# Optimization experiments

Measured on AMD Instinct MI355X. Metric: run time of the kernel, lower is better.

Reference implementation:

```python
import jax, jax.numpy as jnp
import numpy as np
from jax import lax

N_C = 1024  # number of FPS centroids (hard-coded in forward)
K = 32      # knn neighbors (hard-coded in forward)


def _fps(x, far0):
    # Faithful to the source: dist is recomputed against ONLY the latest
    # centroid each iteration (the mask/min-update in the source is dead code),
    # then far = argmax(dist).
    B = x.shape[0]
    bidx = jnp.arange(B)

    def step(far, _):
        c = x[bidx, far]                              # [B, C]
        d = jnp.sum((x - c[:, None, :]) ** 2, -1)     # [B, N]
        return jnp.argmax(d, -1), c

    _, cents = lax.scan(step, far0, None, length=N_C)  # cents: [n_c, B, C]
    return jnp.transpose(cents, (1, 0, 2))             # [B, n_c, C]


def _knn_group(x, cent):
    # squared euclidean distances (same argsort order as torch.cdist)
    d2 = (jnp.sum(cent ** 2, -1)[..., None]
          + jnp.sum(x ** 2, -1)[:, None, :]
          - 2.0 * jnp.einsum('bmc,bnc->bmn', cent, x))   # [B, n_c, N]
    _, idx = lax.top_k(-d2, K)                            # [B, n_c, K] smallest dists
    neighbors = jax.vmap(lambda xb, ib: xb[ib])(x, idx)   # [B, n_c, K, C]
    return neighbors


def _conv1x1(h, w, b):
    # 1x1 Conv1d == channel matmul; h: [B, Cin, L], w: [Cout, Cin]
    return jax.nn.relu(jnp.einsum('oi,bil->bol', w, h) + b[None, :, None])


def setup_inputs() -> dict:
    key = jax.random.key(0)
    ks = jax.random.split(key, 20)
    B, N, C = 4, 16384, 3
    num_classes = 3
    p = lambda k, shp: (jax.random.normal(k, shp, jnp.float32) * 0.02)
    return {
        'x': jax.random.normal(ks[0], (B, N, C), jnp.float32),
        'far_init': jax.random.randint(ks[1], (B,), 0, N, jnp.int32),
        'w1': p(ks[2], (64, 3)),    'b1': p(ks[3], (64,)),
        'w2': p(ks[4], (64, 64)),   'b2': p(ks[5], (64,)),
        'w3': p(ks[6], (64, 64)),   'b3': p(ks[7], (64,)),
        'w4': p(ks[8], (128, 64)),  'b4': p(ks[9], (128,)),
        'w5': p(ks[10], (1024, 128)), 'b5': p(ks[11], (1024,)),
        'fw1': p(ks[12], (512, 1024)), 'fb1': p(ks[13], (512,)),
        'fw2': p(ks[14], (256, 512)),  'fb2': p(ks[15], (256,)),
        'fw3': p(ks[16], (num_classes, 256)), 'fb3': p(ks[17], (num_classes,)),
    }


def reference(x, far_init, w1, b1, w2, b2, w3, b3, w4, b4, w5, b5,
              fw1, fb1, fw2, fb2, fw3, fb3):
    B, N, C = x.shape
    cent = _fps(x, far_init)                 # [B, n_c, C]
    neighbors = _knn_group(x, cent)          # [B, n_c, K, C]
    h = jnp.transpose(neighbors, (0, 3, 1, 2)).reshape(B, C, N_C * K)
    h = _conv1x1(h, w1, b1)
    h = _conv1x1(h, w2, b2)
    h = _conv1x1(h, w3, b3)
    h = _conv1x1(h, w4, b4)
    h = _conv1x1(h, w5, b5)                  # [B, 1024, n_c*K]
    g = jnp.max(h, axis=2)                   # global max pool -> [B, 1024]
    g = jax.nn.relu(g @ fw1.T + fb1)
    g = jax.nn.relu(g @ fw2.T + fb2)
    return g @ fw3.T + fb3                   # [B, num_classes]
```

## Files before the change

kernel.cpp:

```cpp
#include <hip/hip_runtime.h>

#define BN  4
#define NPT 16384
#define NCC 1024
#define KNN 32

#define HBINS    2048
#define CCH      2
#define CAND_CAP 768

#define OFF_CCOUNT 0
#define OFF_SCOUNT 64
#define OFF_SBITS  128
#define OFF_POOL   (128 + BN*(NPT/32)*4)
#define OFF_CLIST  (OFF_POOL + BN*NCC*4)
#define OFF_H1     (OFF_CLIST + BN*NCC*4)
#define OFF_H2     (OFF_H1 + BN*512*4)
#define OFF_SLIST  (OFF_H2 + BN*256*4)

typedef short bf16x8 __attribute__((ext_vector_type(8)));
typedef float f32x4  __attribute__((ext_vector_type(4)));
typedef float f32x2  __attribute__((ext_vector_type(2)));

__device__ __forceinline__ short f2bf(float f) {
    unsigned u = __float_as_uint(f);
    return (short)((u + 0x7fffu + ((u >> 16) & 1u)) >> 16);
}
__device__ __forceinline__ bf16x8 cvt8(const float* __restrict__ p) {
    bf16x8 v;
#pragma unroll
    for (int j = 0; j < 8; ++j) v[j] = f2bf(p[j]);
    return v;
}

__global__ __launch_bounds__(1024) void fps_kernel(const float* __restrict__ x,
    const int* __restrict__ far_init, int* __restrict__ clist, int* __restrict__ ccount,
    int* __restrict__ scount, unsigned* __restrict__ sbits, float* __restrict__ pool)
{
#pragma clang fp contract(off)
    const int b = blockIdx.x, t = threadIdx.x;
    __shared__ __align__(16) unsigned char seen[NPT];
    __shared__ unsigned long long slot[3];

    if (t < 512) sbits[b*(NPT/32) + t] = 0u;
    pool[b*NCC + t] = 0.0f;
    if (t == 0) { ccount[b] = 0; scount[b] = 0; }

    const float* xb = x + (size_t)b * NPT * 3;
    f32x2 px[8], py[8], pz[8];
#pragma unroll
    for (int r = 0; r < 8; ++r) {
        int ia = t + ((2*r) << 10), ib = ia + 1024;
        px[r] = f32x2{xb[ia*3+0], xb[ib*3+0]};
        py[r] = f32x2{xb[ia*3+1], xb[ib*3+1]};
        pz[r] = f32x2{xb[ia*3+2], xb[ib*3+2]};
    }
    ((uint4*)seen)[t] = make_uint4(0,0,0,0);
    if (t == 0) { slot[0] = 0ull; slot[1] = 0ull; slot[2] = 0ull; }
    int prev_bx = far_init[b];
    __syncthreads();
    int pbs = __builtin_amdgcn_readfirstlane(prev_bx);
    float cx = xb[pbs*3], cy = xb[pbs*3+1], cz = xb[pbs*3+2];

    int done = 0;
    for (int it = 0; it < NCC-1; ++it) {
        const int p = it % 3;
        const f32x2 cX = {cx, cx}, cY = {cy, cy}, cZ = {cz, cz};
        float best = -1.0f; int bi = 0;
#pragma unroll
        for (int r = 0; r < 8; ++r) {
            f32x2 dx = px[r] - cX;
            f32x2 dy = py[r] - cY;
            f32x2 dz = pz[r] - cZ;
            f32x2 m1 = dx * dx;
            f32x2 m2 = dy * dy;
            f32x2 m3 = dz * dz;
            f32x2 s  = (m1 + m2) + m3;
            int ia = t + ((2*r) << 10);
            if (s.x > best) { best = s.x; bi = ia; }
            if (s.y > best) { best = s.y; bi = ia + 1024; }
        }
#pragma unroll
        for (int m = 1; m < 64; m <<= 1) {
            float od = __shfl_xor(best, m, 64);
            int   oi = __shfl_xor(bi,   m, 64);
            if (od > best || (od == best && oi < bi)) { best = od; bi = oi; }
        }
        if ((t & 63) == 0) {
            unsigned long long pk =
                (((unsigned long long)__float_as_uint(best)) << 32)
                | (unsigned)(NPT - 1 - bi);
            atomicMax(&slot[p], pk);
        }
        if (t == 0) seen[prev_bx] = 1;
        __syncthreads();
        int bx = NPT - 1 - (int)(unsigned)(slot[p] & 0xFFFFFFFFull);
        if (t == 0) slot[(it + 2) % 3] = 0ull;
        if (seen[bx]) { done = 1; break; }
        prev_bx = bx;
        int bxs = __builtin_amdgcn_readfirstlane(bx);
        cx = xb[bxs*3]; cy = xb[bxs*3+1]; cz = xb[bxs*3+2];
    }
    if (!done && t == 0) seen[prev_bx] = 1;
    __syncthreads();
#pragma unroll
    for (int j = 0; j < 16; ++j) {
        int idx = t + (j << 10);
        if (seen[idx]) {
            int pos = atomicAdd(&ccount[b], 1);
            clist[b * NCC + pos] = idx;
        }
    }
}

__device__ __forceinline__ unsigned key_of(float px, float py, float pz, float xn,
                                           float cx, float cy, float cz, float cn)
{
    float dot = __fadd_rn(__fadd_rn(__fmul_rn(cx,px), __fmul_rn(cy,py)), __fmul_rn(cz,pz));
    float d2  = __fsub_rn(__fadd_rn(cn, xn), __fmul_rn(2.0f, dot));
    unsigned u = __float_as_uint(d2);
    return u ^ ((u >> 31) ? 0xFFFFFFFFu : 0x80000000u);
}

__device__ __forceinline__ void wave_scan_bins(const unsigned* __restrict__ H,
    int nbins, int rem, int lane, int* __restrict__ out_bin, int* __restrict__ out_below)
{
    int per = nbins >> 6;
    int base = lane * per;
    unsigned part = 0;
    for (int q = 0; q < per; ++q) part += H[base + q];
    unsigned inc = part;
#pragma unroll
    for (int m = 1; m < 64; m <<= 1) {
        unsigned u = __shfl_up(inc, m, 64);
        if (lane >= m) inc += u;
    }
    unsigned exc = inc - part;
    unsigned long long mk = __ballot(exc < (unsigned)rem && inc >= (unsigned)rem);
    int src = __ffsll((long long)mk) - 1;
    if (lane == src) {
        unsigned run = exc; int bb = base;
        for (int q = 0; q < per; ++q) {
            unsigned h = H[base + q];
            if (run + h >= (unsigned)rem) { bb = base + q; break; }
            run += h;
        }
        *out_bin = bb; *out_below = (int)run;
    }
}

__global__ __launch_bounds__(1024) void knn_kernel(const float* __restrict__ x,
    const int* __restrict__ clist, const int* __restrict__ ccount,
    unsigned* __restrict__ sbits, int* __restrict__ slist, int* __restrict__ scount)
{
    const int b = blockIdx.y, t = threadIdx.x;
    const int lane = t & 63, w = t >> 6;
    const int cnt = ccount[b];
    const int cbase = blockIdx.x * CCH;
    if (cbase >= cnt) return;
    const float* xb = x + (size_t)b * NPT * 3;

    __shared__ unsigned hist[CCH * HBINS];
    __shared__ unsigned cand[CCH * CAND_CAP];
    __shared__ float cpx[CCH], cpy[CCH], cpz[CCH], cpn[CCH];
    __shared__ unsigned candCnt[CCH];
    __shared__ int s_bb[CCH], s_below[CCH], s_rrem[CCH], s_need[CCH], s_pref[CCH];
    __shared__ unsigned s_tau[CCH];
    __shared__ int s_tbin, s_tbelow;

    if (t < CCH) {
        int ci = clist[b * NCC + min(cbase + t, cnt - 1)];
        float cx = xb[ci*3], cy = xb[ci*3+1], cz = xb[ci*3+2];
        cpx[t] = cx; cpy[t] = cy; cpz[t] = cz;
        cpn[t] = __fadd_rn(__fadd_rn(__fmul_rn(cx,cx), __fmul_rn(cy,cy)), __fmul_rn(cz,cz));
        candCnt[t] = 0;
    }
    for (int i = t; i < CCH * HBINS; i += 1024) hist[i] = 0;
    __syncthreads();

    unsigned keys[NPT/1024][CCH];
#pragma unroll
    for (int j = 0; j < NPT/1024; ++j) {
        int i = t + (j << 10);
        float px = xb[i*3], py = xb[i*3+1], pz = xb[i*3+2];
        float xn = __fadd_rn(__fadd_rn(__fmul_rn(px,px), __fmul_rn(py,py)), __fmul_rn(pz,pz));
#pragma unroll
        for (int c = 0; c < CCH; ++c) {
            unsigned key = key_of(px,py,pz,xn, cpx[c],cpy[c],cpz[c],cpn[c]);
            keys[j][c] = key;
            atomicAdd(&hist[c*HBINS + (key >> 21)], 1u);
        }
    }
    __syncthreads();

    if (w < CCH)
        wave_scan_bins(&hist[w*HBINS], HBINS, KNN, lane, &s_bb[w], &s_below[w]);
    __syncthreads();
    if (t < CCH) s_rrem[t] = KNN - s_below[t];
    __syncthreads();

#pragma unroll
    for (int j = 0; j < NPT/1024; ++j) {
#pragma unroll
        for (int c = 0; c < CCH; ++c) {
            unsigned key = keys[j][c];
            if ((int)(key >> 21) == s_bb[c]) {
                unsigned pos = atomicAdd(&candCnt[c], 1u);
                if (pos < CAND_CAP) cand[c*CAND_CAP + pos] = key;
            }
        }
    }
    __syncthreads();

    if (w < CCH) {
        unsigned cc = candCnt[w];
        if (cc <= CAND_CAP) {
            int r = s_rrem[w] - 1;
            const unsigned* C = &cand[w*CAND_CAP];
            for (int idx = lane; idx < (int)cc; idx += 64) {
                unsigned k = C[idx]; int rank = 0;
                for (int q = 0; q < (int)cc; ++q) {
                    unsigned kq = C[q];
                    rank += (kq < k || (kq == k && q < idx)) ? 1 : 0;
                }
                if (rank == r) s_tau[w] = k;
            }
            if (lane == 0) s_need[w] = 0;
        } else if (lane == 0) s_need[w] = 1;
    }
    __syncthreads();

    for (int c = 0; c < CCH; ++c) {
        if (s_need[c]) {
            const float cx = cpx[c], cy = cpy[c], cz = cpz[c], cn = cpn[c];
            for (int i = t; i < HBINS; i += 1024) hist[i] = 0;
            __syncthreads();
            for (int j = 0; j < NPT/1024; ++j) {
                int i = t + (j << 10);
                float px = xb[i*3], py = xb[i*3+1], pz = xb[i*3+2];
                float xn = __fadd_rn(__fadd_rn(__fmul_rn(px,px), __fmul_rn(py,py)), __fmul_rn(pz,pz));
                unsigned key = key_of(px,py,pz,xn, cx,cy,cz,cn);
                if ((int)(key >> 21) == s_bb[c]) atomicAdd(&hist[(key >> 10) & 2047u], 1u);
            }
            __syncthreads();
            if (w == 0) wave_scan_bins(hist, HBINS, s_rrem[c], lane, &s_tbin, &s_tbelow);
            __syncthreads();
            if (t == 0) { s_pref[c] = (s_bb[c] << 11) | s_tbin; s_rrem[c] -= s_tbelow; }
            __syncthreads();
            for (int i = t; i < 1024; i += 1024) hist[i] = 0;
            __syncthreads();
            for (int j = 0; j < NPT/1024; ++j) {
                int i = t + (j << 10);
                float px = xb[i*3], py = xb[i*3+1], pz = xb[i*3+2];
                float xn = __fadd_rn(__fadd_rn(__fmul_rn(px,px), __fmul_rn(py,py)), __fmul_rn(pz,pz));
                unsigned key = key_of(px,py,pz,xn, cx,cy,cz,cn);
                if ((int)(key >> 10) == s_pref[c]) atomicAdd(&hist[key & 1023u], 1u);
            }
            __syncthreads();
            if (w == 0) wave_scan_bins(hist, 1024, s_rrem[c], lane, &s_tbin, &s_tbelow);
            __syncthreads();
            if (t == 0) s_tau[c] = (((unsigned)s_pref[c]) << 10) | (unsigned)s_tbin;
            __syncthreads();
        }
    }
    __syncthreads();

#pragma unroll
    for (int j = 0; j < NPT/1024; ++j) {
        int i = t + (j << 10);
        bool sel = false;
#pragma unroll
        for (int c = 0; c < CCH; ++c) sel |= (keys[j][c] <= s_tau[c]);
        if (sel) {
            unsigned bit = 1u << (i & 31);
            unsigned old = atomicOr(&sbits[b*(NPT/32) + (i >> 5)], bit);
            if (!(old & bit)) {
                int pos = atomicAdd(&scount[b], 1);
                slist[b * NPT + pos] = i;
            }
        }
    }
}

#define MFMA16(a, bfr, c) __builtin_amdgcn_mfma_f32_16x16x32_bf16(a, bfr, c, 0, 0, 0)

__global__ __launch_bounds__(1024) void mlp_kernel(const float* __restrict__ x,
    const int* __restrict__ sel_list, const int* __restrict__ sel_count,
    const float* __restrict__ w1, const float* __restrict__ b1,
    const float* __restrict__ w2, const float* __restrict__ b2,
    const float* __restrict__ w3, const float* __restrict__ b3,
    const float* __restrict__ w4, const float* __restrict__ b4,
    const float* __restrict__ w5, const float* __restrict__ b5,
    float* __restrict__ pool)
{
    const int b = blockIdx.y, z = blockIdx.z, t = threadIdx.x;
    const int cnt = sel_count[b];
    if ((blockIdx.x << 6) >= cnt) return;
    const int lane = t & 63;
    const int w    = __builtin_amdgcn_readfirstlane(t >> 6);
    const int m    = lane & 15, quad = lane >> 4;

    __shared__ __align__(16) short A1[64 * 72];
    __shared__ __align__(16) short A2[64 * 72];
    __shared__ __align__(16) short A3[64 * 136];
    __shared__ float sx[3 * 64];

    const int ocA = (w >> 2) * 16 + m;
    bf16x8 bw2[2], bw3[2], bw4[2][2], bw5[4];
#pragma unroll
    for (int ks = 0; ks < 2; ++ks) {
        bw2[ks] = cvt8(w2 + ocA*64 + ks*32 + quad*8);
        bw3[ks] = cvt8(w3 + ocA*64 + ks*32 + quad*8);
    }
    int oc4i[2];
#pragma unroll
    for (int r2 = 0; r2 < 2; ++r2) {
        oc4i[r2] = ((w >> 2) + 4*r2) * 16 + m;
#pragma unroll
        for (int ks = 0; ks < 2; ++ks)
            bw4[r2][ks] = cvt8(w4 + oc4i[r2]*64 + ks*32 + quad*8);
    }
    const int oc5 = z*256 + w*16 + m;
#pragma unroll
    for (int ks = 0; ks < 4; ++ks)
        bw5[ks] = cvt8(w5 + oc5*128 + ks*32 + quad*8);
    const float bias2 = b2[ocA], bias3 = b3[ocA];
    const float bias4_0 = b4[oc4i[0]], bias4_1 = b4[oc4i[1]];
    const float bias5 = b5[oc5];
    float w1v[4][3], b1v[4];
#pragma unroll
    for (int i = 0; i < 4; ++i) {
        int oc = w*4 + i;
        w1v[i][0] = w1[oc*3+0]; w1v[i][1] = w1[oc*3+1]; w1v[i][2] = w1[oc*3+2];
        b1v[i] = b1[oc];
    }
    const int pt0 = (w & 3) * 16;

    for (int base = blockIdx.x << 6; base < cnt; base += (32 << 6)) {
        const int npts = min(64, cnt - base);
        __syncthreads();
        if (t < 64) {
            int idx = sel_list[b * NPT + base + min(t, npts - 1)];
            const float* xp = x + ((size_t)b * NPT + idx) * 3;
            sx[t] = xp[0]; sx[64 + t] = xp[1]; sx[128 + t] = xp[2];
        }
        __syncthreads();
        {
            float x0 = sx[lane], x1 = sx[64 + lane], x2 = sx[128 + lane];
#pragma unroll
            for (int i = 0; i < 4; ++i) {
                float acc = fmaf(x2, w1v[i][2], fmaf(x1, w1v[i][1],
                             fmaf(x0, w1v[i][0], b1v[i])));
                A1[lane*72 + w*4 + i] = f2bf(fmaxf(acc, 0.0f));
            }
        }
        __syncthreads();
        {
            bf16x8 a0 = *(const bf16x8*)&A1[(pt0 + m)*72 + quad*8];
            bf16x8 a1 = *(const bf16x8*)&A1[(pt0 + m)*72 + 32 + quad*8];
            f32x4 d = {0.f, 0.f, 0.f, 0.f};
            d = MFMA16(a0, bw2[0], d);
            d = MFMA16(a1, bw2[1], d);
#pragma unroll
            for (int r = 0; r < 4; ++r)
                A2[(pt0 + quad*4 + r)*72 + ocA] = f2bf(fmaxf(d[r] + bias2, 0.0f));
        }
        __syncthreads();
        {
            bf16x8 a0 = *(const bf16x8*)&A2[(pt0 + m)*72 + quad*8];
            bf16x8 a1 = *(const bf16x8*)&A2[(pt0 + m)*72 + 32 + quad*8];
            f32x4 d = {0.f, 0.f, 0.f, 0.f};
            d = MFMA16(a0, bw3[0], d);
            d = MFMA16(a1, bw3[1], d);
#pragma unroll
            for (int r = 0; r < 4; ++r)
                A1[(pt0 + quad*4 + r)*72 + ocA] = f2bf(fmaxf(d[r] + bias3, 0.0f));
        }
        __syncthreads();
        {
            bf16x8 a0 = *(const bf16x8*)&A1[(pt0 + m)*72 + quad*8];
            bf16x8 a1 = *(const bf16x8*)&A1[(pt0 + m)*72 + 32 + quad*8];
#pragma unroll
            for (int r2 = 0; r2 < 2; ++r2) {
                f32x4 d = {0.f, 0.f, 0.f, 0.f};
                d = MFMA16(a0, bw4[r2][0], d);
                d = MFMA16(a1, bw4[r2][1], d);
                float bs = r2 ? bias4_1 : bias4_0;
#pragma unroll
                for (int r = 0; r < 4; ++r)
                    A3[(pt0 + quad*4 + r)*136 + oc4i[r2]] = f2bf(fmaxf(d[r] + bs, 0.0f));
            }
        }
        __syncthreads();
        {
            float vm = 0.0f;
#pragma unroll
            for (int pt4 = 0; pt4 < 4; ++pt4) {
                const int q0 = pt4 * 16;
                f32x4 d = {0.f, 0.f, 0.f, 0.f};
#pragma unroll
                for (int ks = 0; ks < 4; ++ks) {
                    bf16x8 a = *(const bf16x8*)&A3[(q0 + m)*136 + ks*32 + quad*8];
                    d = MFMA16(a, bw5[ks], d);
                }
#pragma unroll
                for (int r = 0; r < 4; ++r)
                    vm = fmaxf(vm, fmaxf(d[r] + bias5, 0.0f));
            }
            vm = fmaxf(vm, __shfl_xor(vm, 16, 64));
            vm = fmaxf(vm, __shfl_xor(vm, 32, 64));
            if (lane < 16)
                atomicMax((int*)&pool[b*NCC + z*256 + w*16 + lane], __float_as_int(vm));
        }
    }
}

__global__ __launch_bounds__(1024) void head1_kernel(const float* __restrict__ pool,
    const float* __restrict__ fw1, const float* __restrict__ fb1,
    float* __restrict__ h1g)
{
    const int bo = blockIdx.x, b = blockIdx.y, t = threadIdx.x;
    const int lane = t & 63, w = t >> 6;
    __shared__ float g[1024];
    g[t] = pool[b*NCC + t];
    __syncthreads();
#pragma unroll
    for (int i = 0; i < 2; ++i) {
        int o = bo * 32 + w * 2 + i;
        float acc = 0.0f;
#pragma unroll
        for (int j = 0; j < 16; ++j) {
            int k = lane + (j << 6);
            acc += g[k] * fw1[o*1024 + k];
        }
#pragma unroll
        for (int m = 1; m < 64; m <<= 1) acc += __shfl_xor(acc, m, 64);
        if (lane == 0) h1g[b*512 + o] = fmaxf(acc + fb1[o], 0.0f);
    }
}

__global__ __launch_bounds__(1024) void head2_kernel(const float* __restrict__ h1g,
    const float* __restrict__ fw2, const float* __restrict__ fb2,
    float* __restrict__ h2g)
{
    const int bo = blockIdx.x, b = blockIdx.y, t = threadIdx.x;
    const int lane = t & 63, w = t >> 6;
    __shared__ float h1[512];
    if (t < 512) h1[t] = h1g[b*512 + t];
    __syncthreads();
#pragma unroll
    for (int i = 0; i < 2; ++i) {
        int o = bo * 32 + w * 2 + i;
        float acc = 0.0f;
#pragma unroll
        for (int j = 0; j < 8; ++j) {
            int k = lane + (j << 6);
            acc += h1[k] * fw2[o*512 + k];
        }
#pragma unroll
        for (int m = 1; m < 64; m <<= 1) acc += __shfl_xor(acc, m, 64);
        if (lane == 0) h2g[b*256 + o] = fmaxf(acc + fb2[o], 0.0f);
    }
}

__global__ __launch_bounds__(256) void head3_kernel(const float* __restrict__ h2g,
    const float* __restrict__ fw3, const float* __restrict__ fb3,
    float* __restrict__ out)
{
    const int b = blockIdx.x, t = threadIdx.x;
    const int lane = t & 63, w = t >> 6;
    __shared__ float h2[256];
    h2[t] = h2g[b*256 + t];
    __syncthreads();
    if (w < 3) {
        float acc = 0.0f;
#pragma unroll
        for (int j = 0; j < 4; ++j) {
            int k = lane + (j << 6);
            acc += h2[k] * fw3[w*256 + k];
        }
#pragma unroll
        for (int m = 1; m < 64; m <<= 1) acc += __shfl_xor(acc, m, 64);
        if (lane == 0) out[b*3 + w] = acc + fb3[w];
    }
}

extern "C" void kernel_launch(void* const* d_in, const int* in_sizes, int n_in,
                              void* d_out, int out_size, void* d_ws, size_t ws_size,
                              hipStream_t stream)
{
    const float* x    = (const float*)d_in[0];
    const int*   far0 = (const int*)  d_in[1];
    const float *w1 = (const float*)d_in[2],  *b1 = (const float*)d_in[3];
    const float *w2 = (const float*)d_in[4],  *b2 = (const float*)d_in[5];
    const float *w3 = (const float*)d_in[6],  *b3 = (const float*)d_in[7];
    const float *w4 = (const float*)d_in[8],  *b4 = (const float*)d_in[9];
    const float *w5 = (const float*)d_in[10], *b5 = (const float*)d_in[11];
    const float *fw1 = (const float*)d_in[12], *fb1 = (const float*)d_in[13];
    const float *fw2 = (const float*)d_in[14], *fb2 = (const float*)d_in[15];
    const float *fw3 = (const float*)d_in[16], *fb3 = (const float*)d_in[17];

    char* ws = (char*)d_ws;
    int*      ccount = (int*)     (ws + OFF_CCOUNT);
    int*      scount = (int*)     (ws + OFF_SCOUNT);
    unsigned* sbits  = (unsigned*)(ws + OFF_SBITS);
    float*    pool   = (float*)   (ws + OFF_POOL);
    int*      clist  = (int*)     (ws + OFF_CLIST);
    float*    h1g    = (float*)   (ws + OFF_H1);
    float*    h2g    = (float*)   (ws + OFF_H2);
    int*      slist  = (int*)     (ws + OFF_SLIST);

    fps_kernel<<<BN, 1024, 0, stream>>>(x, far0, clist, ccount, scount, sbits, pool);
    knn_kernel<<<dim3(NCC/CCH, BN), 1024, 0, stream>>>(x, clist, ccount, sbits, slist, scount);
    mlp_kernel<<<dim3(32, BN, 4), 1024, 0, stream>>>(x, slist, scount,
        w1,b1, w2,b2, w3,b3, w4,b4, w5,b5, pool);
    head1_kernel<<<dim3(16, BN), 1024, 0, stream>>>(pool, fw1, fb1, h1g);
    head2_kernel<<<dim3(8, BN), 1024, 0, stream>>>(h1g, fw2, fb2, h2g);
    head3_kernel<<<BN, 256, 0, stream>>>(h2g, fw3, fb3, (float*)d_out);
}
```

Measured before the change: 158.0 us.

## Fuse all stages into one persistent kernel with software grid barriers

Replaces the six separate launches (FPS, kNN, MLP, three head layers) with a single 64-block persistent kernel that runs each stage in turn, separated by atomic-counter grid barriers in workspace memory. The aim is to remove per-launch overhead and inter-kernel gaps, which matter because the later stages are small. In exchange, kNN and MLP now run on only 64 blocks instead of up to 2048 and 512 blocks, so these stages get much less parallelism. The design also relies on all 64 blocks being resident at once, and it adds a memset launch to reset the barrier counters.

```diff
diff --git a/kernel.cpp b/kernel.cpp
--- a/kernel.cpp
+++ b/kernel.cpp
@@ -8,6 +8,8 @@
 #define HBINS    2048
 #define CCH      2
 #define CAND_CAP 768
+
+#define NBLK 64
 
 #define OFF_CCOUNT 0
 #define OFF_SCOUNT 64
@@ -17,6 +19,7 @@
 #define OFF_H1     (OFF_CLIST + BN*NCC*4)
 #define OFF_H2     (OFF_H1 + BN*512*4)
 #define OFF_SLIST  (OFF_H2 + BN*256*4)
+#define OFF_BAR    (OFF_SLIST + BN*NPT*4)
 
 typedef short bf16x8 __attribute__((ext_vector_type(8)));
 typedef float f32x4  __attribute__((ext_vector_type(4)));
@@ -31,86 +34,6 @@
 #pragma unroll
     for (int j = 0; j < 8; ++j) v[j] = f2bf(p[j]);
     return v;
-}
-
-__global__ __launch_bounds__(1024) void fps_kernel(const float* __restrict__ x,
-    const int* __restrict__ far_init, int* __restrict__ clist, int* __restrict__ ccount,
-    int* __restrict__ scount, unsigned* __restrict__ sbits, float* __restrict__ pool)
-{
-#pragma clang fp contract(off)
-    const int b = blockIdx.x, t = threadIdx.x;
-    __shared__ __align__(16) unsigned char seen[NPT];
-    __shared__ unsigned long long slot[3];
-
-    if (t < 512) sbits[b*(NPT/32) + t] = 0u;
-    pool[b*NCC + t] = 0.0f;
-    if (t == 0) { ccount[b] = 0; scount[b] = 0; }
-
-    const float* xb = x + (size_t)b * NPT * 3;
-    f32x2 px[8], py[8], pz[8];
-#pragma unroll
-    for (int r = 0; r < 8; ++r) {
-        int ia = t + ((2*r) << 10), ib = ia + 1024;
-        px[r] = f32x2{xb[ia*3+0], xb[ib*3+0]};
-        py[r] = f32x2{xb[ia*3+1], xb[ib*3+1]};
-        pz[r] = f32x2{xb[ia*3+2], xb[ib*3+2]};
-    }
-    ((uint4*)seen)[t] = make_uint4(0,0,0,0);
-    if (t == 0) { slot[0] = 0ull; slot[1] = 0ull; slot[2] = 0ull; }
-    int prev_bx = far_init[b];
-    __syncthreads();
-    int pbs = __builtin_amdgcn_readfirstlane(prev_bx);
-    float cx = xb[pbs*3], cy = xb[pbs*3+1], cz = xb[pbs*3+2];
-
-    int done = 0;
-    for (int it = 0; it < NCC-1; ++it) {
-        const int p = it % 3;
-        const f32x2 cX = {cx, cx}, cY = {cy, cy}, cZ = {cz, cz};
-        float best = -1.0f; int bi = 0;
-#pragma unroll
-        for (int r = 0; r < 8; ++r) {
-            f32x2 dx = px[r] - cX;
-            f32x2 dy = py[r] - cY;
-            f32x2 dz = pz[r] - cZ;
-            f32x2 m1 = dx * dx;
-            f32x2 m2 = dy * dy;
-            f32x2 m3 = dz * dz;
-            f32x2 s  = (m1 + m2) + m3;
-            int ia = t + ((2*r) << 10);
-            if (s.x > best) { best = s.x; bi = ia; }
-            if (s.y > best) { best = s.y; bi = ia + 1024; }
-        }
-#pragma unroll
-        for (int m = 1; m < 64; m <<= 1) {
-            float od = __shfl_xor(best, m, 64);
-            int   oi = __shfl_xor(bi,   m, 64);
-            if (od > best || (od == best && oi < bi)) { best = od; bi = oi; }
-        }
-        if ((t & 63) == 0) {
-            unsigned long long pk =
-                (((unsigned long long)__float_as_uint(best)) << 32)
-                | (unsigned)(NPT - 1 - bi);
-            atomicMax(&slot[p], pk);
-        }
-        if (t == 0) seen[prev_bx] = 1;
-        __syncthreads();
-        int bx = NPT - 1 - (int)(unsigned)(slot[p] & 0xFFFFFFFFull);
-        if (t == 0) slot[(it + 2) % 3] = 0ull;
-        if (seen[bx]) { done = 1; break; }
-        prev_bx = bx;
-        int bxs = __builtin_amdgcn_readfirstlane(bx);
-        cx = xb[bxs*3]; cy = xb[bxs*3+1]; cz = xb[bxs*3+2];
-    }
-    if (!done && t == 0) seen[prev_bx] = 1;
-    __syncthreads();
-#pragma unroll
-    for (int j = 0; j < 16; ++j) {
-        int idx = t + (j << 10);
-        if (seen[idx]) {
-            int pos = atomicAdd(&ccount[b], 1);
-            clist[b * NCC + pos] = idx;
-        }
-    }
 }
 
 __device__ __forceinline__ unsigned key_of(float px, float py, float pz, float xn,
@@ -149,339 +72,450 @@
     }
 }
 
-__global__ __launch_bounds__(1024) void knn_kernel(const float* __restrict__ x,
-    const int* __restrict__ clist, const int* __restrict__ ccount,
-    unsigned* __restrict__ sbits, int* __restrict__ slist, int* __restrict__ scount)
-{
-    const int b = blockIdx.y, t = threadIdx.x;
-    const int lane = t & 63, w = t >> 6;
-    const int cnt = ccount[b];
-    const int cbase = blockIdx.x * CCH;
-    if (cbase >= cnt) return;
-    const float* xb = x + (size_t)b * NPT * 3;
-
-    __shared__ unsigned hist[CCH * HBINS];
-    __shared__ unsigned cand[CCH * CAND_CAP];
-    __shared__ float cpx[CCH], cpy[CCH], cpz[CCH], cpn[CCH];
-    __shared__ unsigned candCnt[CCH];
-    __shared__ int s_bb[CCH], s_below[CCH], s_rrem[CCH], s_need[CCH], s_pref[CCH];
-    __shared__ unsigned s_tau[CCH];
-    __shared__ int s_tbin, s_tbelow;
-
-    if (t < CCH) {
-        int ci = clist[b * NCC + min(cbase + t, cnt - 1)];
-        float cx = xb[ci*3], cy = xb[ci*3+1], cz = xb[ci*3+2];
-        cpx[t] = cx; cpy[t] = cy; cpz[t] = cz;
-        cpn[t] = __fadd_rn(__fadd_rn(__fmul_rn(cx,cx), __fmul_rn(cy,cy)), __fmul_rn(cz,cz));
-        candCnt[t] = 0;
-    }
-    for (int i = t; i < CCH * HBINS; i += 1024) hist[i] = 0;
+__device__ __forceinline__ void gridbar(unsigned* __restrict__ bar, int ph) {
+    __threadfence();
     __syncthreads();
-
-    unsigned keys[NPT/1024][CCH];
-#pragma unroll
-    for (int j = 0; j < NPT/1024; ++j) {
-        int i = t + (j << 10);
-        float px = xb[i*3], py = xb[i*3+1], pz = xb[i*3+2];
-        float xn = __fadd_rn(__fadd_rn(__fmul_rn(px,px), __fmul_rn(py,py)), __fmul_rn(pz,pz));
-#pragma unroll
-        for (int c = 0; c < CCH; ++c) {
-            unsigned key = key_of(px,py,pz,xn, cpx[c],cpy[c],cpz[c],cpn[c]);
-            keys[j][c] = key;
-            atomicAdd(&hist[c*HBINS + (key >> 21)], 1u);
-        }
+    if (threadIdx.x == 0) {
+        __hip_atomic_fetch_add(&bar[ph], 1u, __ATOMIC_RELEASE, __HIP_MEMORY_SCOPE_AGENT);
+        while (__hip_atomic_load(&bar[ph], __ATOMIC_ACQUIRE, __HIP_MEMORY_SCOPE_AGENT)
+               < (unsigned)NBLK)
+            __builtin_amdgcn_s_sleep(8);
     }
     __syncthreads();
-
-    if (w < CCH)
-        wave_scan_bins(&hist[w*HBINS], HBINS, KNN, lane, &s_bb[w], &s_below[w]);
-    __syncthreads();
-    if (t < CCH) s_rrem[t] = KNN - s_below[t];
-    __syncthreads();
-
-#pragma unroll
-    for (int j = 0; j < NPT/1024; ++j) {
-#pragma unroll
-        for (int c = 0; c < CCH; ++c) {
-            unsigned key = keys[j][c];
-            if ((int)(key >> 21) == s_bb[c]) {
-                unsigned pos = atomicAdd(&candCnt[c], 1u);
-                if (pos < CAND_CAP) cand[c*CAND_CAP + pos] = key;
-            }
-        }
-    }
-    __syncthreads();
-
-    if (w < CCH) {
-        unsigned cc = candCnt[w];
-        if (cc <= CAND_CAP) {
-            int r = s_rrem[w] - 1;
-            const unsigned* C = &cand[w*CAND_CAP];
-            for (int idx = lane; idx < (int)cc; idx += 64) {
-                unsigned k = C[idx]; int rank = 0;
-                for (int q = 0; q < (int)cc; ++q) {
-                    unsigned kq = C[q];
-                    rank += (kq < k || (kq == k && q < idx)) ? 1 : 0;
-                }
-                if (rank == r) s_tau[w] = k;
-            }
-            if (lane == 0) s_need[w] = 0;
-        } else if (lane == 0) s_need[w] = 1;
-    }
-    __syncthreads();
-
-    for (int c = 0; c < CCH; ++c) {
-        if (s_need[c]) {
-            const float cx = cpx[c], cy = cpy[c], cz = cpz[c], cn = cpn[c];
-            for (int i = t; i < HBINS; i += 1024) hist[i] = 0;
-            __syncthreads();
-            for (int j = 0; j < NPT/1024; ++j) {
-                int i = t + (j << 10);
-                float px = xb[i*3], py = xb[i*3+1], pz = xb[i*3+2];
-                float xn = __fadd_rn(__fadd_rn(__fmul_rn(px,px), __fmul_rn(py,py)), __fmul_rn(pz,pz));
-                unsigned key = key_of(px,py,pz,xn, cx,cy,cz,cn);
-                if ((int)(key >> 21) == s_bb[c]) atomicAdd(&hist[(key >> 10) & 2047u], 1u);
-            }
-            __syncthreads();
-            if (w == 0) wave_scan_bins(hist, HBINS, s_rrem[c], lane, &s_tbin, &s_tbelow);
-            __syncthreads();
-            if (t == 0) { s_pref[c] = (s_bb[c] << 11) | s_tbin; s_rrem[c] -= s_tbelow; }
-            __syncthreads();
-            for (int i = t; i < 1024; i += 1024) hist[i] = 0;
-            __syncthreads();
-            for (int j = 0; j < NPT/1024; ++j) {
-                int i = t + (j << 10);
-                float px = xb[i*3], py = xb[i*3+1], pz = xb[i*3+2];
-                float xn = __fadd_rn(__fadd_rn(__fmul_rn(px,px), __fmul_rn(py,py)), __fmul_rn(pz,pz));
-                unsigned key = key_of(px,py,pz,xn, cx,cy,cz,cn);
-                if ((int)(key >> 10) == s_pref[c]) atomicAdd(&hist[key & 1023u], 1u);
-            }
-            __syncthreads();
-            if (w == 0) wave_scan_bins(hist, 1024, s_rrem[c], lane, &s_tbin, &s_tbelow);
-            __syncthreads();
-            if (t == 0) s_tau[c] = (((unsigned)s_pref[c]) << 10) | (unsigned)s_tbin;
-            __syncthreads();
-        }
-    }
-    __syncthreads();
-
-#pragma unroll
-    for (int j = 0; j < NPT/1024; ++j) {
-        int i = t + (j << 10);
-        bool sel = false;
-#pragma unroll
-        for (int c = 0; c < CCH; ++c) sel |= (keys[j][c] <= s_tau[c]);
-        if (sel) {
-            unsigned bit = 1u << (i & 31);
-            unsigned old = atomicOr(&sbits[b*(NPT/32) + (i >> 5)], bit);
-            if (!(old & bit)) {
-                int pos = atomicAdd(&scount[b], 1);
-                slist[b * NPT + pos] = i;
-            }
-        }
-    }
+    __threadfence();
 }
 
 #define MFMA16(a, bfr, c) __builtin_amdgcn_mfma_f32_16x16x32_bf16(a, bfr, c, 0, 0, 0)
 
-__global__ __launch_bounds__(1024) void mlp_kernel(const float* __restrict__ x,
-    const int* __restrict__ sel_list, const int* __restrict__ sel_count,
+__global__ __launch_bounds__(1024) void mega_kernel(const float* __restrict__ x,
+    const int* __restrict__ far_init,
     const float* __restrict__ w1, const float* __restrict__ b1,
     const float* __restrict__ w2, const float* __restrict__ b2,
     const float* __restrict__ w3, const float* __restrict__ b3,
     const float* __restrict__ w4, const float* __restrict__ b4,
     const float* __restrict__ w5, const float* __restrict__ b5,
-    float* __restrict__ pool)
+    const float* __restrict__ fw1, const float* __restrict__ fb1,
+    const float* __restrict__ fw2, const float* __restrict__ fb2,
+    const float* __restrict__ fw3, const float* __restrict__ fb3,
+    int* __restrict__ clist, int* __restrict__ ccount, int* __restrict__ scount,
+    unsigned* __restrict__ sbits, int* __restrict__ slist, float* __restrict__ pool,
+    float* __restrict__ h1g, float* __restrict__ h2g, float* __restrict__ out,
+    unsigned* __restrict__ bar)
 {
-    const int b = blockIdx.y, z = blockIdx.z, t = threadIdx.x;
-    const int cnt = sel_count[b];
-    if ((blockIdx.x << 6) >= cnt) return;
-    const int lane = t & 63;
-    const int w    = __builtin_amdgcn_readfirstlane(t >> 6);
-    const int m    = lane & 15, quad = lane >> 4;
-
-    __shared__ __align__(16) short A1[64 * 72];
-    __shared__ __align__(16) short A2[64 * 72];
-    __shared__ __align__(16) short A3[64 * 136];
-    __shared__ float sx[3 * 64];
-
-    const int ocA = (w >> 2) * 16 + m;
-    bf16x8 bw2[2], bw3[2], bw4[2][2], bw5[4];
-#pragma unroll
-    for (int ks = 0; ks < 2; ++ks) {
-        bw2[ks] = cvt8(w2 + ocA*64 + ks*32 + quad*8);
-        bw3[ks] = cvt8(w3 + ocA*64 + ks*32 + quad*8);
-    }
-    int oc4i[2];
-#pragma unroll
-    for (int r2 = 0; r2 < 2; ++r2) {
-        oc4i[r2] = ((w >> 2) + 4*r2) * 16 + m;
-#pragma unroll
-        for (int ks = 0; ks < 2; ++ks)
-            bw4[r2][ks] = cvt8(w4 + oc4i[r2]*64 + ks*32 + quad*8);
-    }
-    const int oc5 = z*256 + w*16 + m;
-#pragma unroll
-    for (int ks = 0; ks < 4; ++ks)
-        bw5[ks] = cvt8(w5 + oc5*128 + ks*32 + quad*8);
-    const float bias2 = b2[ocA], bias3 = b3[ocA];
-    const float bias4_0 = b4[oc4i[0]], bias4_1 = b4[oc4i[1]];
-    const float bias5 = b5[oc5];
-    float w1v[4][3], b1v[4];
-#pragma unroll
-    for (int i = 0; i < 4; ++i) {
-        int oc = w*4 + i;
-        w1v[i][0] = w1[oc*3+0]; w1v[i][1] = w1[oc*3+1]; w1v[i][2] = w1[oc*3+2];
-        b1v[i] = b1[oc];
-    }
-    const int pt0 = (w & 3) * 16;
-
-    for (int base = blockIdx.x << 6; base < cnt; base += (32 << 6)) {
-        const int npts = min(64, cnt - base);
+    const int blk = blockIdx.x, t = threadIdx.x;
+    __shared__ __align__(16) char smem[36864];
+
+    {
+#pragma clang fp contract(off)
+        if (blk < 4) {
+            const int b = blk;
+            unsigned char* seen = (unsigned char*)smem;
+            unsigned long long* slot = (unsigned long long*)(smem + 16384);
+
+            if (t < 512) sbits[b*(NPT/32) + t] = 0u;
+            pool[b*NCC + t] = 0.0f;
+            if (t == 0) { ccount[b] = 0; scount[b] = 0; }
+
+            const float* xb = x + (size_t)b * NPT * 3;
+            f32x2 px[8], py[8], pz[8];
+#pragma unroll
+            for (int r = 0; r < 8; ++r) {
+                int ia = t + ((2*r) << 10), ib = ia + 1024;
+                px[r] = f32x2{xb[ia*3+0], xb[ib*3+0]};
+                py[r] = f32x2{xb[ia*3+1], xb[ib*3+1]};
+                pz[r] = f32x2{xb[ia*3+2], xb[ib*3+2]};
+            }
+            ((uint4*)seen)[t] = make_uint4(0,0,0,0);
+            if (t == 0) { slot[0] = 0ull; slot[1] = 0ull; slot[2] = 0ull; }
+            int prev_bx = far_init[b];
+            __syncthreads();
+            int pbs = __builtin_amdgcn_readfirstlane(prev_bx);
+            float cx = xb[pbs*3], cy = xb[pbs*3+1], cz = xb[pbs*3+2];
+
+            int done = 0;
+            for (int it = 0; it < NCC-1; ++it) {
+                const int p = it % 3;
+                const f32x2 cX = {cx, cx}, cY = {cy, cy}, cZ = {cz, cz};
+                float best = -1.0f; int bi = 0;
+#pragma unroll
+                for (int r = 0; r < 8; ++r) {
+                    f32x2 dx = px[r] - cX;
+                    f32x2 dy = py[r] - cY;
+                    f32x2 dz = pz[r] - cZ;
+                    f32x2 m1 = dx * dx;
+                    f32x2 m2 = dy * dy;
+                    f32x2 m3 = dz * dz;
+                    f32x2 s  = (m1 + m2) + m3;
+                    int ia = t + ((2*r) << 10);
+                    if (s.x > best) { best = s.x; bi = ia; }
+                    if (s.y > best) { best = s.y; bi = ia + 1024; }
+                }
+#pragma unroll
+                for (int m = 1; m < 64; m <<= 1) {
+                    float od = __shfl_xor(best, m, 64);
+                    int   oi = __shfl_xor(bi,   m, 64);
+                    if (od > best || (od == best && oi < bi)) { best = od; bi = oi; }
+                }
+                if ((t & 63) == 0) {
+                    unsigned long long pk =
+                        (((unsigned long long)__float_as_uint(best)) << 32)
+                        | (unsigned)(NPT - 1 - bi);
+                    atomicMax(&slot[p], pk);
+                }
+                if (t == 0) seen[prev_bx] = 1;
+                __syncthreads();
+                int bx = NPT - 1 - (int)(unsigned)(slot[p] & 0xFFFFFFFFull);
+                if (t == 0) slot[(it + 2) % 3] = 0ull;
+                if (seen[bx]) { done = 1; break; }
+                prev_bx = bx;
+                int bxs = __builtin_amdgcn_readfirstlane(bx);
+                cx = xb[bxs*3]; cy = xb[bxs*3+1]; cz = xb[bxs*3+2];
+            }
+            if (!done && t == 0) seen[prev_bx] = 1;
+            __syncthreads();
+#pragma unroll
+            for (int j = 0; j < 16; ++j) {
+                int idx = t + (j << 10);
+                if (seen[idx]) {
+                    int pos = atomicAdd(&ccount[b], 1);
+                    clist[b * NCC + pos] = idx;
+                }
+            }
+        }
+    }
+    gridbar(bar, 0);
+
+    {
+        const int c0 = ccount[0], c1 = ccount[1], c2 = ccount[2], c3 = ccount[3];
+        const int maxc = max(max(c0,c1), max(c2,c3));
+        unsigned* hist    = (unsigned*)smem;
+        unsigned* cand    = (unsigned*)(smem + 16384);
+        float*    cpx     = (float*)(smem + 22528);
+        float*    cpy     = cpx + CCH;
+        float*    cpz     = cpy + CCH;
+        float*    cpn     = cpz + CCH;
+        unsigned* candCnt = (unsigned*)(cpn + CCH);
+        int*      s_bb    = (int*)(candCnt + CCH);
+        int*      s_below = s_bb + CCH;
+        int*      s_rrem  = s_below + CCH;
+        int*      s_need  = s_rrem + CCH;
+        int*      s_pref  = s_need + CCH;
+        unsigned* s_tau   = (unsigned*)(s_pref + CCH);
+        int*      s_tb    = (int*)(s_tau + CCH);
+
+        const int lane = t & 63, w = t >> 6;
+
+        for (int wi = blk; (wi >> 2) * CCH < maxc; wi += NBLK) {
+            const int b = wi & 3;
+            const int cnt = (b==0) ? c0 : (b==1) ? c1 : (b==2) ? c2 : c3;
+            const int cbase = (wi >> 2) * CCH;
+            if (cbase >= cnt) continue;
+            const float* xb = x + (size_t)b * NPT * 3;
+
+            __syncthreads();
+            if (t < CCH) {
+                int ci = clist[b * NCC + min(cbase + t, cnt - 1)];
+                float cx = xb[ci*3], cy = xb[ci*3+1], cz = xb[ci*3+2];
+                cpx[t] = cx; cpy[t] = cy; cpz[t] = cz;
+                cpn[t] = __fadd_rn(__fadd_rn(__fmul_rn(cx,cx), __fmul_rn(cy,cy)), __fmul_rn(cz,cz));
+                candCnt[t] = 0;
+            }
+            for (int i = t; i < CCH * HBINS; i += 1024) hist[i] = 0;
+            __syncthreads();
+
+            unsigned keys[NPT/1024][CCH];
+#pragma unroll
+            for (int j = 0; j < NPT/1024; ++j) {
+                int i = t + (j << 10);
+                float px = xb[i*3], py = xb[i*3+1], pz = xb[i*3+2];
+                float xn = __fadd_rn(__fadd_rn(__fmul_rn(px,px), __fmul_rn(py,py)), __fmul_rn(pz,pz));
+#pragma unroll
+                for (int c = 0; c < CCH; ++c) {
+                    unsigned key = key_of(px,py,pz,xn, cpx[c],cpy[c],cpz[c],cpn[c]);
+                    keys[j][c] = key;
+                    atomicAdd(&hist[c*HBINS + (key >> 21)], 1u);
+                }
+            }
+            __syncthreads();
+
+            if (w < CCH)
+                wave_scan_bins(&hist[w*HBINS], HBINS, KNN, lane, &s_bb[w], &s_below[w]);
+            __syncthreads();
+            if (t < CCH) s_rrem[t] = KNN - s_below[t];
+            __syncthreads();
+
+#pragma unroll
+            for (int j = 0; j < NPT/1024; ++j) {
+#pragma unroll
+                for (int c = 0; c < CCH; ++c) {
+                    unsigned key = keys[j][c];
+                    if ((int)(key >> 21) == s_bb[c]) {
+                        unsigned pos = atomicAdd(&candCnt[c], 1u);
+                        if (pos < CAND_CAP) cand[c*CAND_CAP + pos] = key;
+                    }
+                }
+            }
+            __syncthreads();
+
+            if (w < CCH) {
+                unsigned cc = candCnt[w];
+                if (cc <= CAND_CAP) {
+                    int r = s_rrem[w] - 1;
+                    const unsigned* C = &cand[w*CAND_CAP];
+                    for (int idx = lane; idx < (int)cc; idx += 64) {
+                        unsigned k = C[idx]; int rank = 0;
+                        for (int q = 0; q < (int)cc; ++q) {
+                            unsigned kq = C[q];
+                            rank += (kq < k || (kq == k && q < idx)) ? 1 : 0;
+                        }
+                        if (rank == r) s_tau[w] = k;
+                    }
+                    if (lane == 0) s_need[w] = 0;
+                } else if (lane == 0) s_need[w] = 1;
+            }
+            __syncthreads();
+
+            for (int c = 0; c < CCH; ++c) {
+                if (s_need[c]) {
+                    const float cx = cpx[c], cy = cpy[c], cz = cpz[c], cn = cpn[c];
+                    for (int i = t; i < HBINS; i += 1024) hist[i] = 0;
+                    __syncthreads();
+                    for (int j = 0; j < NPT/1024; ++j) {
+                        int i = t + (j << 10);
+                        float px = xb[i*3], py = xb[i*3+1], pz = xb[i*3+2];
+                        float xn = __fadd_rn(__fadd_rn(__fmul_rn(px,px), __fmul_rn(py,py)), __fmul_rn(pz,pz));
+                        unsigned key = key_of(px,py,pz,xn, cx,cy,cz,cn);
+                        if ((int)(key >> 21) == s_bb[c]) atomicAdd(&hist[(key >> 10) & 2047u], 1u);
+                    }
+                    __syncthreads();
+                    if (w == 0) wave_scan_bins(hist, HBINS, s_rrem[c], lane, &s_tb[0], &s_tb[1]);
+                    __syncthreads();
+                    if (t == 0) { s_pref[c] = (s_bb[c] << 11) | s_tb[0]; s_rrem[c] -= s_tb[1]; }
+                    __syncthreads();
+                    for (int i = t; i < 1024; i += 1024) hist[i] = 0;
+                    __syncthreads();
+                    for (int j = 0; j < NPT/1024; ++j) {
+                        int i = t + (j << 10);
+                        float px = xb[i*3], py = xb[i*3+1], pz = xb[i*3+2];
+                        float xn = __fadd_rn(__fadd_rn(__fmul_rn(px,px), __fmul_rn(py,py)), __fmul_rn(pz,pz));
+                        unsigned key = key_of(px,py,pz,xn, cx,cy,cz,cn);
+                        if ((int)(key >> 10) == s_pref[c]) atomicAdd(&hist[key & 1023u], 1u);
+                    }
+                    __syncthreads();
+                    if (w == 0) wave_scan_bins(hist, 1024, s_rrem[c], lane, &s_tb[0], &s_tb[1]);
+                    __syncthreads();
+                    if (t == 0) s_tau[c] = (((unsigned)s_pref[c]) << 10) | (unsigned)s_tb[0];
+                    __syncthreads();
+                }
+            }
+            __syncthreads();
+
+#pragma unroll
+            for (int j = 0; j < NPT/1024; ++j) {
+                int i = t + (j << 10);
+                bool sel = false;
+#pragma unroll
+                for (int c = 0; c < CCH; ++c) sel |= (keys[j][c] <= s_tau[c]);
+                if (sel) {
+                    unsigned bit = 1u << (i & 31);
+                    unsigned old = atomicOr(&sbits[b*(NPT/32) + (i >> 5)], bit);
+                    if (!(old & bit)) {
+                        int pos = atomicAdd(&scount[b], 1);
+                        slist[b * NPT + pos] = i;
+                    }
+                }
+            }
+        }
+    }
+    gridbar(bar, 1);
+
+    {
+        const int s0 = scount[0], s1 = scount[1], s2 = scount[2], s3 = scount[3];
+        short* A1 = (short*)smem;
+        short* A2 = (short*)(smem + 9216);
+        short* A3 = (short*)(smem + 18432);
+        float* sx = (float*)(smem + 35840);
+
+        const int lane = t & 63;
+        const int w    = __builtin_amdgcn_readfirstlane(t >> 6);
+        const int m    = lane & 15, quad = lane >> 4;
+        const int b    = blk & 3;
+        const int z    = (blk >> 2) & 3;
+        const int cnt  = (b==0) ? s0 : (b==1) ? s1 : (b==2) ? s2 : s3;
+
+        const int ocA = (w >> 2) * 16 + m;
+        bf16x8 bw2[2], bw3[2], bw4[2][2], bw5[4];
+#pragma unroll
+        for (int ks = 0; ks < 2; ++ks) {
+            bw2[ks] = cvt8(w2 + ocA*64 + ks*32 + quad*8);
+            bw3[ks] = cvt8(w3 + ocA*64 + ks*32 + quad*8);
+        }
+        int oc4i[2];
+#pragma unroll
+        for (int r2 = 0; r2 < 2; ++r2) {
+            oc4i[r2] = ((w >> 2) + 4*r2) * 16 + m;
+#pragma unroll
+            for (int ks = 0; ks < 2; ++ks)
+                bw4[r2][ks] = cvt8(w4 + oc4i[r2]*64 + ks*32 + quad*8);
+        }
+        const int oc5 = z*256 + w*16 + m;
+#pragma unroll
+        for (int ks = 0; ks < 4; ++ks)
+            bw5[ks] = cvt8(w5 + oc5*128 + ks*32 + quad*8);
+        const float bias2 = b2[ocA], bias3 = b3[ocA];
+        const float bias4_0 = b4[oc4i[0]], bias4_1 = b4[oc4i[1]];
+        const float bias5 = b5[oc5];
+        float w1v[4][3], b1v[4];
+#pragma unroll
+        for (int i = 0; i < 4; ++i) {
+            int oc = w*4 + i;
+            w1v[i][0] = w1[oc*3+0]; w1v[i][1] = w1[oc*3+1]; w1v[i][2] = w1[oc*3+2];
+            b1v[i] = b1[oc];
+        }
+        const int pt0 = (w & 3) * 16;
+
+        for (int xblk = blk >> 4; xblk * 64 < cnt; xblk += 4) {
+            const int base = xblk << 6;
+            const int npts = min(64, cnt - base);
+            __syncthreads();
+            if (t < 64) {
+                int idx = slist[b * NPT + base + min(t, npts - 1)];
+                const float* xp = x + ((size_t)b * NPT + idx) * 3;
+                sx[t] = xp[0]; sx[64 + t] = xp[1]; sx[128 + t] = xp[2];
+            }
+            __syncthreads();
+            {
+                float x0 = sx[lane], x1 = sx[64 + lane], x2 = sx[128 + lane];
+#pragma unroll
+                for (int i = 0; i < 4; ++i) {
+                    float acc = fmaf(x2, w1v[i][2], fmaf(x1, w1v[i][1],
+                                 fmaf(x0, w1v[i][0], b1v[i])));
+                    A1[lane*72 + w*4 + i] = f2bf(fmaxf(acc, 0.0f));
+                }
+            }
+            __syncthreads();
+            {
+                bf16x8 a0 = *(const bf16x8*)&A1[(pt0 + m)*72 + quad*8];
+                bf16x8 a1 = *(const bf16x8*)&A1[(pt0 + m)*72 + 32 + quad*8];
+                f32x4 d = {0.f, 0.f, 0.f, 0.f};
+                d = MFMA16(a0, bw2[0], d);
+                d = MFMA16(a1, bw2[1], d);
+#pragma unroll
+                for (int r = 0; r < 4; ++r)
+                    A2[(pt0 + quad*4 + r)*72 + ocA] = f2bf(fmaxf(d[r] + bias2, 0.0f));
+            }
+            __syncthreads();
+            {
+                bf16x8 a0 = *(const bf16x8*)&A2[(pt0 + m)*72 + quad*8];
+                bf16x8 a1 = *(const bf16x8*)&A2[(pt0 + m)*72 + 32 + quad*8];
+                f32x4 d = {0.f, 0.f, 0.f, 0.f};
+                d = MFMA16(a0, bw3[0], d);
+                d = MFMA16(a1, bw3[1], d);
+#pragma unroll
+                for (int r = 0; r < 4; ++r)
+                    A1[(pt0 + quad*4 + r)*72 + ocA] = f2bf(fmaxf(d[r] + bias3, 0.0f));
+            }
+            __syncthreads();
+            {
+                bf16x8 a0 = *(const bf16x8*)&A1[(pt0 + m)*72 + quad*8];
+                bf16x8 a1 = *(const bf16x8*)&A1[(pt0 + m)*72 + 32 + quad*8];
+#pragma unroll
+                for (int r2 = 0; r2 < 2; ++r2) {
+                    f32x4 d = {0.f, 0.f, 0.f, 0.f};
+                    d = MFMA16(a0, bw4[r2][0], d);
+                    d = MFMA16(a1, bw4[r2][1], d);
+                    float bs = r2 ? bias4_1 : bias4_0;
+#pragma unroll
+                    for (int r = 0; r < 4; ++r)
+                        A3[(pt0 + quad*4 + r)*136 + oc4i[r2]] = f2bf(fmaxf(d[r] + bs, 0.0f));
+                }
+            }
+            __syncthreads();
+            {
+                float vm = 0.0f;
+#pragma unroll
+                for (int pt4 = 0; pt4 < 4; ++pt4) {
+                    const int q0 = pt4 * 16;
+                    f32x4 d = {0.f, 0.f, 0.f, 0.f};
+#pragma unroll
+                    for (int ks = 0; ks < 4; ++ks) {
+                        bf16x8 a = *(const bf16x8*)&A3[(q0 + m)*136 + ks*32 + quad*8];
+                        d = MFMA16(a, bw5[ks], d);
+                    }
+#pragma unroll
+                    for (int r = 0; r < 4; ++r)
+                        vm = fmaxf(vm, fmaxf(d[r] + bias5, 0.0f));
+                }
+                vm = fmaxf(vm, __shfl_xor(vm, 16, 64));
+                vm = fmaxf(vm, __shfl_xor(vm, 32, 64));
+                if (lane < 16)
+                    atomicMax((int*)&pool[b*NCC + z*256 + w*16 + lane], __float_as_int(vm));
+            }
+        }
+    }
+    gridbar(bar, 2);
+
+    {
+        const int bo = blk >> 2, b = blk & 3;
+        const int lane = t & 63, w = t >> 6;
+        float* g = (float*)smem;
+        g[t] = pool[b*NCC + t];
         __syncthreads();
-        if (t < 64) {
-            int idx = sel_list[b * NPT + base + min(t, npts - 1)];
-            const float* xp = x + ((size_t)b * NPT + idx) * 3;
-            sx[t] = xp[0]; sx[64 + t] = xp[1]; sx[128 + t] = xp[2];
-        }
+#pragma unroll
+        for (int i = 0; i < 2; ++i) {
+            int o = bo * 32 + w * 2 + i;
+            float acc = 0.0f;
+#pragma unroll
+            for (int j = 0; j < 16; ++j) {
+                int k = lane + (j << 6);
+                acc += g[k] * fw1[o*1024 + k];
+            }
+#pragma unroll
+            for (int m = 1; m < 64; m <<= 1) acc += __shfl_xor(acc, m, 64);
+            if (lane == 0) h1g[b*512 + o] = fmaxf(acc + fb1[o], 0.0f);
+        }
+    }
+    gridbar(bar, 3);
+
+    if (blk < 32) {
+        const int bo = blk >> 2, b = blk & 3;
+        const int lane = t & 63, w = t >> 6;
+        float* h1 = (float*)smem;
+        if (t < 512) h1[t] = h1g[b*512 + t];
         __syncthreads();
-        {
-            float x0 = sx[lane], x1 = sx[64 + lane], x2 = sx[128 + lane];
-#pragma unroll
-            for (int i = 0; i < 4; ++i) {
-                float acc = fmaf(x2, w1v[i][2], fmaf(x1, w1v[i][1],
-                             fmaf(x0, w1v[i][0], b1v[i])));
-                A1[lane*72 + w*4 + i] = f2bf(fmaxf(acc, 0.0f));
-            }
-        }
+#pragma unroll
+        for (int i = 0; i < 2; ++i) {
+            int o = bo * 32 + w * 2 + i;
+            float acc = 0.0f;
+#pragma unroll
+            for (int j = 0; j < 8; ++j) {
+                int k = lane + (j << 6);
+                acc += h1[k] * fw2[o*512 + k];
+            }
+#pragma unroll
+            for (int m = 1; m < 64; m <<= 1) acc += __shfl_xor(acc, m, 64);
+            if (lane == 0) h2g[b*256 + o] = fmaxf(acc + fb2[o], 0.0f);
+        }
+    }
+    gridbar(bar, 4);
+
+    if (blk < 4) {
+        const int b = blk;
+        const int lane = t & 63, w = t >> 6;
+        float* h2 = (float*)smem;
+        if (t < 256) h2[t] = h2g[b*256 + t];
         __syncthreads();
-        {
-            bf16x8 a0 = *(const bf16x8*)&A1[(pt0 + m)*72 + quad*8];
-            bf16x8 a1 = *(const bf16x8*)&A1[(pt0 + m)*72 + 32 + quad*8];
-            f32x4 d = {0.f, 0.f, 0.f, 0.f};
-            d = MFMA16(a0, bw2[0], d);
-            d = MFMA16(a1, bw2[1], d);
-#pragma unroll
-            for (int r = 0; r < 4; ++r)
-                A2[(pt0 + quad*4 + r)*72 + ocA] = f2bf(fmaxf(d[r] + bias2, 0.0f));
-        }
-        __syncthreads();
-        {
-            bf16x8 a0 = *(const bf16x8*)&A2[(pt0 + m)*72 + quad*8];
-            bf16x8 a1 = *(const bf16x8*)&A2[(pt0 + m)*72 + 32 + quad*8];
-            f32x4 d = {0.f, 0.f, 0.f, 0.f};
-            d = MFMA16(a0, bw3[0], d);
-            d = MFMA16(a1, bw3[1], d);
-#pragma unroll
-            for (int r = 0; r < 4; ++r)
-                A1[(pt0 + quad*4 + r)*72 + ocA] = f2bf(fmaxf(d[r] + bias3, 0.0f));
-        }
-        __syncthreads();
-        {
-            bf16x8 a0 = *(const bf16x8*)&A1[(pt0 + m)*72 + quad*8];
-            bf16x8 a1 = *(const bf16x8*)&A1[(pt0 + m)*72 + 32 + quad*8];
-#pragma unroll
-            for (int r2 = 0; r2 < 2; ++r2) {
-                f32x4 d = {0.f, 0.f, 0.f, 0.f};
-                d = MFMA16(a0, bw4[r2][0], d);
-                d = MFMA16(a1, bw4[r2][1], d);
-                float bs = r2 ? bias4_1 : bias4_0;
-#pragma unroll
-                for (int r = 0; r < 4; ++r)
-                    A3[(pt0 + quad*4 + r)*136 + oc4i[r2]] = f2bf(fmaxf(d[r] + bs, 0.0f));
-            }
-        }
-        __syncthreads();
-        {
-            float vm = 0.0f;
-#pragma unroll
-            for (int pt4 = 0; pt4 < 4; ++pt4) {
-                const int q0 = pt4 * 16;
-                f32x4 d = {0.f, 0.f, 0.f, 0.f};
-#pragma unroll
-                for (int ks = 0; ks < 4; ++ks) {
-                    bf16x8 a = *(const bf16x8*)&A3[(q0 + m)*136 + ks*32 + quad*8];
-                    d = MFMA16(a, bw5[ks], d);
-                }
-#pragma unroll
-                for (int r = 0; r < 4; ++r)
-                    vm = fmaxf(vm, fmaxf(d[r] + bias5, 0.0f));
-            }
-            vm = fmaxf(vm, __shfl_xor(vm, 16, 64));
-            vm = fmaxf(vm, __shfl_xor(vm, 32, 64));
-            if (lane < 16)
-                atomicMax((int*)&pool[b*NCC + z*256 + w*16 + lane], __float_as_int(vm));
-        }
-    }
-}
-
-__global__ __launch_bounds__(1024) void head1_kernel(const float* __restrict__ pool,
-    const float* __restrict__ fw1, const float* __restrict__ fb1,
-    float* __restrict__ h1g)
-{
-    const int bo = blockIdx.x, b = blockIdx.y, t = threadIdx.x;
-    const int lane = t & 63, w = t >> 6;
-    __shared__ float g[1024];
-    g[t] = pool[b*NCC + t];
-    __syncthreads();
-#pragma unroll
-    for (int i = 0; i < 2; ++i) {
-        int o = bo * 32 + w * 2 + i;
-        float acc = 0.0f;
-#pragma unroll
-        for (int j = 0; j < 16; ++j) {
-            int k = lane + (j << 6);
-            acc += g[k] * fw1[o*1024 + k];
-        }
-#pragma unroll
-        for (int m = 1; m < 64; m <<= 1) acc += __shfl_xor(acc, m, 64);
-        if (lane == 0) h1g[b*512 + o] = fmaxf(acc + fb1[o], 0.0f);
-    }
-}
-
-__global__ __launch_bounds__(1024) void head2_kernel(const float* __restrict__ h1g,
-    const float* __restrict__ fw2, const float* __restrict__ fb2,
-    float* __restrict__ h2g)
-{
-    const int bo = blockIdx.x, b = blockIdx.y, t = threadIdx.x;
-    const int lane = t & 63, w = t >> 6;
-    __shared__ float h1[512];
-    if (t < 512) h1[t] = h1g[b*512 + t];
-    __syncthreads();
-#pragma unroll
-    for (int i = 0; i < 2; ++i) {
-        int o = bo * 32 + w * 2 + i;
-        float acc = 0.0f;
-#pragma unroll
-        for (int j = 0; j < 8; ++j) {
-            int k = lane + (j << 6);
-            acc += h1[k] * fw2[o*512 + k];
-        }
-#pragma unroll
-        for (int m = 1; m < 64; m <<= 1) acc += __shfl_xor(acc, m, 64);
-        if (lane == 0) h2g[b*256 + o] = fmaxf(acc + fb2[o], 0.0f);
-    }
-}
-
-__global__ __launch_bounds__(256) void head3_kernel(const float* __restrict__ h2g,
-    const float* __restrict__ fw3, const float* __restrict__ fb3,
-    float* __restrict__ out)
-{
-    const int b = blockIdx.x, t = threadIdx.x;
-    const int lane = t & 63, w = t >> 6;
-    __shared__ float h2[256];
-    h2[t] = h2g[b*256 + t];
-    __syncthreads();
-    if (w < 3) {
-        float acc = 0.0f;
-#pragma unroll
-        for (int j = 0; j < 4; ++j) {
-            int k = lane + (j << 6);
-            acc += h2[k] * fw3[w*256 + k];
-        }
-#pragma unroll
-        for (int m = 1; m < 64; m <<= 1) acc += __shfl_xor(acc, m, 64);
-        if (lane == 0) out[b*3 + w] = acc + fb3[w];
+        if (t < 256 && w < 3) {
+            float acc = 0.0f;
+#pragma unroll
+            for (int j = 0; j < 4; ++j) {
+                int k = lane + (j << 6);
+                acc += h2[k] * fw3[w*256 + k];
+            }
+#pragma unroll
+            for (int m = 1; m < 64; m <<= 1) acc += __shfl_xor(acc, m, 64);
+            if (lane == 0) out[b*3 + w] = acc + fb3[w];
+        }
     }
 }
 
@@ -509,12 +543,10 @@
     float*    h1g    = (float*)   (ws + OFF_H1);
     float*    h2g    = (float*)   (ws + OFF_H2);
     int*      slist  = (int*)     (ws + OFF_SLIST);
-
-    fps_kernel<<<BN, 1024, 0, stream>>>(x, far0, clist, ccount, scount, sbits, pool);
-    knn_kernel<<<dim3(NCC/CCH, BN), 1024, 0, stream>>>(x, clist, ccount, sbits, slist, scount);
-    mlp_kernel<<<dim3(32, BN, 4), 1024, 0, stream>>>(x, slist, scount,
-        w1,b1, w2,b2, w3,b3, w4,b4, w5,b5, pool);
-    head1_kernel<<<dim3(16, BN), 1024, 0, stream>>>(pool, fw1, fb1, h1g);
-    head2_kernel<<<dim3(8, BN), 1024, 0, stream>>>(h1g, fw2, fb2, h2g);
-    head3_kernel<<<BN, 256, 0, stream>>>(h2g, fw3, fb3, (float*)d_out);
-}
+    unsigned* bar    = (unsigned*)(ws + OFF_BAR);
+
+    hipMemsetAsync(bar, 0, 8 * sizeof(unsigned), stream);
+    mega_kernel<<<NBLK, 1024, 0, stream>>>(x, far0,
+        w1,b1, w2,b2, w3,b3, w4,b4, w5,b5, fw1,fb1, fw2,fb2, fw3,fb3,
+        clist, ccount, scount, sbits, slist, pool, h1g, h2g, (float*)d_out, bar);
+}
```

Result: slower. 317.9 us (+101.2%).
